# Optimization experiments

Hardware: AMD Instinct MI355X
Metric: run time of the kernel (lower is better)

The kernel has to match this reference:

```python
import jax, jax.numpy as jnp
import numpy as np

N, E, B = 524288, 4194304, 16384
F_IN, FP, TV, GOUT = 14, 1024, 256, 32
EPS = 1e-5
SLOPE = 0.2  # PyG GATConv default negative_slope


def setup_inputs() -> dict:
    key = jax.random.key(0)
    ks = iter(jax.random.split(key, 64))
    def nrm(shape, scale=1.0):
        return jax.random.normal(next(ks), shape, dtype=jnp.float32) * scale
    def uni(shape, lo, hi):
        return jax.random.uniform(next(ks), shape, dtype=jnp.float32, minval=lo, maxval=hi)
    def bn(d):  # [gamma, beta, running_mean, running_var]
        return jnp.stack([uni((d,), 0.5, 1.5), nrm((d,), 0.1), nrm((d,), 0.1), uni((d,), 0.5, 1.5)])
    return {
        'x': nrm((N, F_IN)),
        'edge_index': jax.random.randint(next(ks), (2, E), 0, N, dtype=jnp.int32),
        'batch': jnp.sort(jax.random.randint(next(ks), (N,), 0, B, dtype=jnp.int32)),
        'fingerprint': nrm((B, FP)),
        'transformer_features': nrm((B, TV)),
        'W1': nrm((F_IN, F_IN), 0.3), 'a_src1': nrm((F_IN,), 0.3), 'a_dst1': nrm((F_IN,), 0.3), 'b1': nrm((F_IN,), 0.1),
        'W2': nrm((F_IN, GOUT), 0.3), 'a_src2': nrm((GOUT,), 0.3), 'a_dst2': nrm((GOUT,), 0.3), 'b2': nrm((GOUT,), 0.1),
        'fc1_w': nrm((FP, 400), 0.04), 'fc1_b': nrm((400,), 0.1), 'bn1': bn(400),
        'fc2_w': nrm((400, 200), 0.07), 'fc2_b': nrm((200,), 0.1), 'bn2': bn(200),
        'fc3_w': nrm((TV, 400), 0.08), 'fc3_b': nrm((400,), 0.1), 'bn3': bn(400),
        'fc4_w': nrm((400, 200), 0.07), 'fc4_b': nrm((200,), 0.1), 'bn4': bn(200),
        'fcc1_w': nrm((GOUT + 400, 100), 0.07), 'fcc1_b': nrm((100,), 0.1), 'bnc': bn(100),
        'fcc2_w': nrm((100, 1), 0.1), 'fcc2_b': nrm((1,), 0.1),
    }


def _bn(h, p):  # eval-mode BatchNorm1d with packed params [4, d]
    return (h - p[2]) * jax.lax.rsqrt(p[3] + EPS) * p[0] + p[1]


def _gat(x, W, a_s, a_d, b, src, dst, n):
    # PyG GATConv, heads=1: messages flow src -> dst, softmax over incoming edges per dst
    h = x @ W                                   # [n, C]
    e = jax.nn.leaky_relu((h @ a_s)[src] + (h @ a_d)[dst], SLOPE)  # [E_tot]
    m = jax.lax.stop_gradient(jax.ops.segment_max(e, dst, num_segments=n))
    w = jnp.exp(e - m[dst])
    denom = jax.ops.segment_sum(w, dst, num_segments=n)
    alpha = w / denom[dst]
    out = jax.ops.segment_sum(alpha[:, None] * h[src], dst, num_segments=n)
    return out + b


def reference(x, edge_index, batch, fingerprint, transformer_features,
              W1, a_src1, a_dst1, b1, W2, a_src2, a_dst2, b2,
              fc1_w, fc1_b, bn1, fc2_w, fc2_b, bn2,
              fc3_w, fc3_b, bn3, fc4_w, fc4_b, bn4,
              fcc1_w, fcc1_b, bnc, fcc2_w, fcc2_b):
    n = x.shape[0]
    loop = jnp.arange(n, dtype=edge_index.dtype)  # add_self_loops
    src = jnp.concatenate([edge_index[0], loop])
    dst = jnp.concatenate([edge_index[1], loop])
    g = jax.nn.relu(_gat(x, W1, a_src1, a_dst1, b1, src, dst, n))
    g = jax.nn.relu(_gat(g, W2, a_src2, a_dst2, b2, src, dst, n))
    pool = jax.ops.segment_sum(g, batch, num_segments=B)  # global_add_pool -> [B, GOUT]
    fp = jax.nn.relu(_bn(fingerprint @ fc1_w + fc1_b, bn1))
    fp = jax.nn.relu(_bn(fp @ fc2_w + fc2_b, bn2))
    tv = jax.nn.relu(_bn(transformer_features @ fc3_w + fc3_b, bn3))
    tv = jax.nn.relu(_bn(tv @ fc4_w + fc4_b, bn4))
    comb = jnp.concatenate([pool, fp, tv], axis=1)  # [B, 32+200+200]
    comb = jax.nn.relu(_bn(comb @ fcc1_w + fcc1_b, bnc))
    return comb @ fcc2_w + fcc2_b  # [B, 1]
```

## Files before the change

### kernel.cpp

```cpp
#include <hip/hip_runtime.h>

typedef unsigned short u16;
typedef unsigned int u32;
typedef __attribute__((ext_vector_type(8))) short bf16x8;
typedef __attribute__((ext_vector_type(4))) float f32x4;

#define N_NODES 524288
#define N_EDGES 4194304
#define N_GRAPH 16384
#define P_BLOCKS 1024
#define BKTS 512
#define DPB 1024
#define CAP 8960
#define TTOT 2825

__device__ __forceinline__ float bf2f(u16 u){ u32 x=((u32)u)<<16; float f; __builtin_memcpy(&f,&x,4); return f; }
__device__ __forceinline__ float lo2f(u32 u){ u32 x=u<<16; float f; __builtin_memcpy(&f,&x,4); return f; }
__device__ __forceinline__ float hi2f(u32 u){ u32 x=u&0xffff0000u; float f; __builtin_memcpy(&f,&x,4); return f; }
__device__ __forceinline__ u16 f2bf(float f){ u32 x; __builtin_memcpy(&x,&f,4); return (u16)((x + 0x7fffu + ((x>>16)&1u))>>16); }
__device__ __forceinline__ float lrelu(float e){ return e>0.f? e : 0.2f*e; }
__device__ __forceinline__ float gload(const void* p, int i, int is32){
    return is32 ? ((const float*)p)[i] : bf2f(((const u16*)p)[i]);
}
__device__ __forceinline__ u32 fmax_key(float f){ u32 u; __builtin_memcpy(&u,&f,4); return (u>>31)? ~u : (u|0x80000000u); }
__device__ __forceinline__ float key_fmax(u32 k){ u32 u = (k>>31)? (k^0x80000000u) : ~k; float f; __builtin_memcpy(&f,&u,4); return f; }

__device__ __forceinline__ void edge_acc(uint4 q0, uint4 q1, float adv, float M,
        float* acc, float& den){
    float as_; __builtin_memcpy(&as_, &q1.w, 4);
    float w = __expf(lrelu(as_ + adv) - M); den += w;
    u32 u[7] = {q0.x,q0.y,q0.z,q0.w,q1.x,q1.y,q1.z};
    #pragma unroll
    for (int f=0;f<14;f++){ u32 uu=u[f>>1]; acc[f] += w*((f&1)? hi2f(uu):lo2f(uu)); }
}

__device__ __forceinline__ void walk8(const int* __restrict__ ssrc, const u16* __restrict__ hsrc,
        int beg, int end, float adv, float M, float* acc, float& den){
    for (int j = beg; j < end; j += 8){
        int s8[8];
        #pragma unroll
        for (int k=0;k<8;k++){
            int e = j + k;
            s8[k] = __builtin_nontemporal_load(ssrc + ((e < end) ? e : (end-1)));
        }
        uint4 r0[8], r1[8];
        #pragma unroll
        for (int k=0;k<8;k++){
            const uint4* hp = (const uint4*)(hsrc + (size_t)s8[k]*16);
            r0[k] = hp[0]; r1[k] = hp[1];
        }
        int m = end - j;
        #pragma unroll
        for (int k=0;k<8;k++) if (k < m) edge_acc(r0[k], r1[k], adv, M, acc, den);
    }
}

__device__ __forceinline__ void gemm_block(u16 (*As)[40], u16 (*Bs)[40],
        const void* __restrict__ A, const u16* __restrict__ Wt,
        const void* __restrict__ bias, const void* __restrict__ bnp, void* __restrict__ out,
        int K, int Kp, int Nc, int ostride, int ooff, int do_relu,
        int out32, int araw, int is32, int bm, int bn, int t){
    int af32 = araw && is32;
    int lane = t & 63, wave = t >> 6;
    int mt = (wave & 1) * 64, nt = (wave >> 1) * 64;
    int quad = lane >> 4, fr = lane & 15;

    f32x4 zero = {0.f, 0.f, 0.f, 0.f};
    f32x4 acc[4][4];
    #pragma unroll
    for (int i=0;i<4;i++)
        #pragma unroll
        for (int j=0;j<4;j++) acc[i][j] = zero;

    int srow0 = t >> 2;
    int scol = (t & 3) * 8;

    for (int k0 = 0; k0 < Kp; k0 += 32){
        #pragma unroll
        for (int h2_=0; h2_<2; h2_++){
            int row = srow0 + h2_*64;
            int gk = k0 + scol;
            uint4 av = make_uint4(0,0,0,0);
            if (gk + 8 <= K){
                if (af32){
                    const float* ap = (const float*)A + (size_t)(bm+row)*K + gk;
                    float4 a0 = *(const float4*)ap, a1 = *(const float4*)(ap+4);
                    av.x = (u32)f2bf(a0.x) | ((u32)f2bf(a0.y)<<16);
                    av.y = (u32)f2bf(a0.z) | ((u32)f2bf(a0.w)<<16);
                    av.z = (u32)f2bf(a1.x) | ((u32)f2bf(a1.y)<<16);
                    av.w = (u32)f2bf(a1.z) | ((u32)f2bf(a1.w)<<16);
                } else {
                    av = *(const uint4*)((const u16*)A + (size_t)(bm+row)*K + gk);
                }
            }
            *(uint4*)(&As[row][scol]) = av;
            uint4 bv = make_uint4(0,0,0,0);
            if (bn + row < Nc) bv = *(const uint4*)(Wt + (size_t)(bn+row)*Kp + gk);
            *(uint4*)(&Bs[row][scol]) = bv;
        }
        __syncthreads();
        bf16x8 af[4], bfr[4];
        #pragma unroll
        for (int i=0;i<4;i++) af[i] = *(const bf16x8*)(&As[mt + i*16 + fr][quad*8]);
        #pragma unroll
        for (int j=0;j<4;j++) bfr[j] = *(const bf16x8*)(&Bs[nt + j*16 + fr][quad*8]);
        #pragma unroll
        for (int i=0;i<4;i++)
            #pragma unroll
            for (int j=0;j<4;j++)
                acc[i][j] = __builtin_amdgcn_mfma_f32_16x16x32_bf16(af[i], bfr[j], acc[i][j], 0, 0, 0);
        __syncthreads();
    }

    #pragma unroll
    for (int j=0;j<4;j++){
        int gn = bn + nt + j*16 + fr;
        if (gn >= Nc) continue;
        float bb = gload(bias, gn, is32);
        float scale = 1.f, shift = bb;
        if (bnp){
            float gm_ = gload(bnp, gn, is32), bt = gload(bnp, Nc+gn, is32);
            float mn = gload(bnp, 2*Nc+gn, is32), vr = gload(bnp, 3*Nc+gn, is32);
            scale = gm_ * rsqrtf(vr + 1e-5f);
            shift = (bb - mn)*scale + bt;
        }
        #pragma unroll
        for (int i=0;i<4;i++){
            #pragma unroll
            for (int r=0;r<4;r++){
                int gm = bm + mt + i*16 + quad*4 + r;
                float v = acc[i][j][r]*scale + shift;
                if (do_relu) v = fmaxf(v, 0.f);
                size_t oidx = (size_t)gm*ostride + ooff + gn;
                if (out32) ((float*)out)[oidx] = v;
                else       ((u16*)out)[oidx] = f2bf(v);
            }
        }
    }
}

__global__ __launch_bounds__(256) void k_detect(const u32* __restrict__ x, int* __restrict__ flag,
        const void* __restrict__ W2, const void* __restrict__ asw, const void* __restrict__ adw,
        float* __restrict__ prep){
    __shared__ int cnt, s32;
    int t = threadIdx.x;
    if (t==0) cnt = 0;
    __syncthreads();
    int c = 0;
    for (int i = t; i < 1024; i += 256){
        u32 e = (x[i] >> 7) & 0xFF;
        if (e >= 110 && e <= 140) c++;
    }
    atomicAdd(&cnt, c);
    __syncthreads();
    if (t==0){ int f = (cnt < 512) ? 1 : 0; *flag = f; s32 = f; }
    __syncthreads();
    int is32 = s32;
    if (t < 28){
        int j = t % 14, which = t / 14;
        const void* av = which ? adw : asw;
        float s = 0.f;
        #pragma unroll
        for (int k=0;k<32;k++) s += gload(W2, j*32+k, is32) * gload(av, k, is32);
        prep[which*14 + j] = s;
    }
}

__global__ __launch_bounds__(256) void k_p1t(const int* __restrict__ dst, u32* __restrict__ tbl_bm,
        const void* __restrict__ Wa, const void* __restrict__ Wb, const void* __restrict__ Wc,
        const void* __restrict__ Wd, const void* __restrict__ We,
        u16* __restrict__ Ta, u16* __restrict__ Tb, u16* __restrict__ Tc,
        u16* __restrict__ Td, u16* __restrict__ Te, const int* __restrict__ flag){
    __shared__ u32 lh[BKTS];
    int bid = blockIdx.x, t = threadIdx.x;
    if (bid >= P_BLOCKS){
        int is32 = *flag;
        int loc = (bid - P_BLOCKS)*256 + t;
        const int n1=400*1024, n2=200*416, n3=400*256, n4=200*416, n5=100*448;
        const void* W; u16* T; int K, Kp, Nc;
        if (loc < n1){ W=Wa; T=Ta; K=1024; Kp=1024; Nc=400; }
        else if ((loc-=n1) < n2){ W=Wb; T=Tb; K=400; Kp=416; Nc=200; }
        else if ((loc-=n2) < n3){ W=Wc; T=Tc; K=256; Kp=256; Nc=400; }
        else if ((loc-=n3) < n4){ W=Wd; T=Td; K=400; Kp=416; Nc=200; }
        else if ((loc-=n4) < n5){ W=We; T=Te; K=432; Kp=448; Nc=100; }
        else return;
        int n = loc / Kp, k = loc - n*Kp;
        T[loc] = (k < K) ? f2bf(gload(W, k*Nc + n, is32)) : (u16)0;
        return;
    }
    int blk = bid;
    lh[t] = 0; lh[t+256] = 0;
    __syncthreads();
    int base = blk*4096;
    #pragma unroll
    for (int k=0;k<16;k++){
        int d = __builtin_nontemporal_load(dst + base + k*256 + t) & (N_NODES-1);
        atomicAdd(&lh[d>>10], 1);
    }
    __syncthreads();
    tbl_bm[blk*BKTS + t]       = lh[t];
    tbl_bm[blk*BKTS + t + 256] = lh[t+256];
}

__global__ __launch_bounds__(256) void k_ttbl(const u32* __restrict__ bm, u32* __restrict__ km){
    __shared__ u32 tile[32][33];
    int bx = blockIdx.x, by = blockIdx.y;
    int tx = threadIdx.x & 31, ty = threadIdx.x >> 5;
    #pragma unroll
    for (int r=0;r<32;r+=8)
        tile[ty+r][tx] = bm[(bx*32 + ty + r)*BKTS + by*32 + tx];
    __syncthreads();
    #pragma unroll
    for (int r=0;r<32;r+=8)
        km[(by*32 + ty + r)*P_BLOCKS + bx*32 + tx] = tile[tx][ty+r];
}

__global__ __launch_bounds__(256) void k_scan1(int* __restrict__ data, int* __restrict__ bsums){
    __shared__ int sh[256];
    int b = blockIdx.x, t = threadIdx.x;
    int base = b*1024 + t*4;
    int4 v = *(const int4*)(data + base);
    int s = v.x+v.y+v.z+v.w;
    sh[t] = s; __syncthreads();
    for (int off=1; off<256; off<<=1){
        int xv = (t>=off)? sh[t-off] : 0; __syncthreads();
        sh[t] += xv; __syncthreads();
    }
    int excl = sh[t] - s;
    if (t==255) bsums[b] = sh[255];
    int4 o; o.x = excl; o.y = excl+v.x; o.z = o.y+v.y; o.w = o.z+v.z;
    *(int4*)(data + base) = o;
}

__global__ __launch_bounds__(256) void k_scan2(int* __restrict__ bsums){
    __shared__ int sh[256];
    int t = threadIdx.x;
    int v0 = bsums[2*t], v1 = bsums[2*t+1];
    int s = v0+v1; sh[t] = s; __syncthreads();
    for (int off=1; off<256; off<<=1){
        int xv = (t>=off)? sh[t-off] : 0; __syncthreads();
        sh[t] += xv; __syncthreads();
    }
    int excl = sh[t] - s;
    bsums[2*t] = excl; bsums[2*t+1] = excl + v0;
}

__global__ __launch_bounds__(256) void k_scan3(int* __restrict__ scan, const int* __restrict__ bsums, int N_, int E_){
    int i = blockIdx.x*256 + threadIdx.x;
    if (i < N_) scan[i] += bsums[i>>10];
    if (i == 0) scan[N_] = E_;
}

__global__ __launch_bounds__(256) void k_p2(const int* __restrict__ src, const int* __restrict__ dst,
        const u32* __restrict__ km, u32* __restrict__ btab){
    __shared__ u32 lh[BKTS], lofs[BKTS], gofs[BKTS];
    __shared__ u32 stage[4096], tgt[4096];
    __shared__ u32 red[256];
    int t = threadIdx.x, blk = blockIdx.x;
    lh[t] = 0; lh[t+256] = 0;
    __syncthreads();
    u32 pr[16], rk[16]; u16 bk[16];
    int base = blk*4096;
    #pragma unroll
    for (int k=0;k<16;k++){
        int e = base + k*256 + t;
        int d = __builtin_nontemporal_load(dst+e) & (N_NODES-1);
        int s = __builtin_nontemporal_load(src+e) & (N_NODES-1);
        u32 b = (u32)d >> 10;
        bk[k] = (u16)b;
        pr[k] = (u32)(d & 1023) | ((u32)s << 10);
        rk[k] = atomicAdd(&lh[b], 1);
    }
    gofs[t]       = km[(size_t)t*P_BLOCKS + blk];
    gofs[t+256]   = km[(size_t)(t+256)*P_BLOCKS + blk];
    __syncthreads();
    u32 v0 = lh[2*t], v1 = lh[2*t+1];
    u32 s2 = v0+v1; red[t] = s2; __syncthreads();
    for (int off=1; off<256; off<<=1){
        u32 xv = (t>=off)? red[t-off] : 0; __syncthreads();
        red[t] += xv; __syncthreads();
    }
    u32 excl = red[t] - s2;
    lofs[2*t] = excl; lofs[2*t+1] = excl + v0;
    __syncthreads();
    #pragma unroll
    for (int k=0;k<16;k++){
        u32 p = lofs[bk[k]] + rk[k];
        stage[p] = pr[k];
        tgt[p]   = gofs[bk[k]] + rk[k];
    }
    __syncthreads();
    #pragma unroll
    for (int k=0;k<16;k++){
        int j = k*256 + t;
        btab[tgt[j]] = stage[j];
    }
}

__global__ __launch_bounds__(256) void k_p3(const u32* __restrict__ km, const u32* __restrict__ btab,
        int* __restrict__ rowptr, int* __restrict__ ssrc){
    __shared__ u32 fh[DPB], fo[DPB];
    __shared__ u32 red[256];
    __shared__ int sst[CAP];
    int t = threadIdx.x, b = blockIdx.x;
    u32 basep = km[(size_t)b*P_BLOCKS];
    u32 endp  = km[(size_t)(b+1)*P_BLOCKS];
    int cnt = (int)(endp - basep);
    #pragma unroll
    for (int i=t;i<DPB;i+=256) fh[i] = 0;
    __syncthreads();
    for (int j=t; j<cnt; j+=256){
        u32 p = btab[basep + j];
        atomicAdd(&fh[p & 1023], 1);
    }
    __syncthreads();
    u32 v0=fh[4*t], v1=fh[4*t+1], v2=fh[4*t+2], v3=fh[4*t+3];
    u32 s4 = v0+v1+v2+v3; red[t] = s4; __syncthreads();
    for (int off=1; off<256; off<<=1){
        u32 xv = (t>=off)? red[t-off] : 0; __syncthreads();
        red[t] += xv; __syncthreads();
    }
    u32 excl = red[t] - s4;
    fo[4*t]=excl; fo[4*t+1]=excl+v0; fo[4*t+2]=excl+v0+v1; fo[4*t+3]=excl+v0+v1+v2;
    __syncthreads();
    #pragma unroll
    for (int i=t;i<DPB;i+=256) rowptr[b*DPB + i] = (int)(basep + fo[i]);
    if (b == BKTS-1 && t == 0) rowptr[N_NODES] = (int)endp;
    __syncthreads();
    for (int j=t; j<cnt; j+=256){
        u32 p = btab[basep + j];
        u32 pos = atomicAdd(&fo[p & 1023], 1);
        if (pos < (u32)CAP) sst[pos] = (int)(p >> 10);
    }
    __syncthreads();
    for (int j=t; j<cnt; j+=256) ssrc[basep + j] = sst[j];
}

__global__ __launch_bounds__(256) void k_linear1(const void* __restrict__ x,
        const void* __restrict__ W1, const void* __restrict__ asw, const void* __restrict__ adw,
        u16* __restrict__ h1, float* __restrict__ ad1, u32* __restrict__ gkey,
        const int* __restrict__ flag){
    int is32 = *flag;
    __shared__ float Wf[196], av[14], dv[14];
    __shared__ float red[256];
    int t = threadIdx.x;
    if (t < 196) Wf[t] = gload(W1, t, is32);
    else if (t < 210) av[t-196] = gload(asw, t-196, is32);
    else if (t < 224) dv[t-210] = gload(adw, t-210, is32);
    __syncthreads();
    int i = blockIdx.x*256 + t;
    float xv[14];
    if (is32){
        const float* xr = (const float*)x + (size_t)i*14;
        #pragma unroll
        for (int k=0;k<14;k++) xv[k] = xr[k];
    } else {
        const u32* xr = (const u32*)((const u16*)x + (size_t)i*14);
        #pragma unroll
        for (int p=0;p<7;p++){ u32 u = xr[p]; xv[2*p]=lo2f(u); xv[2*p+1]=hi2f(u); }
    }
    float h[14];
    #pragma unroll
    for (int j=0;j<14;j++){ float s=0.f;
        #pragma unroll
        for (int k=0;k<14;k++) s += xv[k]*Wf[k*14+j];
        h[j]=s; }
    float a=0.f, d=0.f;
    #pragma unroll
    for (int j=0;j<14;j++){ a += h[j]*av[j]; d += h[j]*dv[j]; }
    ad1[i]=d;
    u32 ou[8];
    #pragma unroll
    for (int p=0;p<7;p++) ou[p] = (u32)f2bf(h[2*p]) | ((u32)f2bf(h[2*p+1])<<16);
    __builtin_memcpy(&ou[7], &a, 4);
    uint4* hp = (uint4*)(h1 + (size_t)i*16);
    hp[0] = make_uint4(ou[0],ou[1],ou[2],ou[3]);
    hp[1] = make_uint4(ou[4],ou[5],ou[6],ou[7]);
    red[t] = a; __syncthreads();
    for (int o=128;o;o>>=1){ if (t<o) red[t]=fmaxf(red[t],red[t+o]); __syncthreads(); }
    if (t==0) atomicMax(gkey, fmax_key(red[0]));
}

__global__ __launch_bounds__(256) void k_g1mlp(const int* __restrict__ rowptr, const int* __restrict__ ssrc,
        const u16* __restrict__ h1, const float* __restrict__ ad1, const u32* __restrict__ gkey1,
        const void* __restrict__ b1, const float* __restrict__ prep,
        u16* __restrict__ g1, float* __restrict__ ad2, u32* __restrict__ gkey2,
        const int* __restrict__ flag,
        const void* __restrict__ fing, const u16* __restrict__ Wt1,
        const void* __restrict__ fc1b, const void* __restrict__ bn1, u16* __restrict__ fp1,
        const void* __restrict__ tv, const u16* __restrict__ Wt3,
        const void* __restrict__ fc3b, const void* __restrict__ bn3, u16* __restrict__ tv1){
    __shared__ u16 As[128][40];
    __shared__ u16 Bs[128][40];
    __shared__ float b1s[14], vas[14], vds[14];
    __shared__ float red[256];
    int is32 = *flag;
    int bid = blockIdx.x, t = threadIdx.x;
    if (bid % 3 == 0){
        int g = bid / 3;
        int gg = (g < 512) ? g : g - 512;
        int r = gg & 7, q = gg >> 3;
        int bn = (q & 3) * 128;
        int bm = ((q >> 2) * 8 + r) * 128;
        if (g < 512)
            gemm_block(As, Bs, fing, Wt1, fc1b, bn1, fp1, 1024, 1024, 400, 400, 0, 1, 0,
                       1, is32, bm, bn, t);
        else
            gemm_block(As, Bs, tv, Wt3, fc3b, bn3, tv1, 256, 256, 400, 400, 0, 1, 0,
                       1, is32, bm, bn, t);
        return;
    }
    int gb = bid - bid/3 - 1;
    if (t < 14) b1s[t] = gload(b1, t, is32);
    else if (t < 28) vas[t-14] = prep[t-14];
    else if (t < 42) vds[t-28] = prep[t-28+14];
    __syncthreads();
    int i = gb*256 + t;
    float adv = ad1[i];
    float M = lrelu(key_fmax(*gkey1) + adv);
    int beg = rowptr[i], end = rowptr[i+1];
    float acc[14] = {0,0,0,0,0,0,0,0,0,0,0,0,0,0};
    float den = 0.f;
    {
        const uint4* hp = (const uint4*)(h1 + (size_t)i*16);
        edge_acc(hp[0], hp[1], adv, M, acc, den);
    }
    walk8(ssrc, h1, beg, end, adv, M, acc, den);
    float inv = 1.0f/den;
    float v[14];
    #pragma unroll
    for (int f=0;f<14;f++) v[f] = fmaxf(acc[f]*inv + b1s[f], 0.f);
    float a2=0.f, d2=0.f;
    #pragma unroll
    for (int f=0;f<14;f++){ a2 += v[f]*vas[f]; d2 += v[f]*vds[f]; }
    ad2[i] = d2;
    u32 ou[8];
    #pragma unroll
    for (int p=0;p<7;p++) ou[p] = (u32)f2bf(v[2*p]) | ((u32)f2bf(v[2*p+1])<<16);
    __builtin_memcpy(&ou[7], &a2, 4);
    uint4* gp = (uint4*)(g1 + (size_t)i*16);
    gp[0]=make_uint4(ou[0],ou[1],ou[2],ou[3]);
    gp[1]=make_uint4(ou[4],ou[5],ou[6],ou[7]);
    red[t] = a2; __syncthreads();
    for (int o=128;o;o>>=1){ if (t<o) red[t]=fmaxf(red[t],red[t+o]); __syncthreads(); }
    if (t==0) atomicMax(gkey2, fmax_key(red[0]));
}

__global__ __launch_bounds__(256) void k_g2mlp(const int* __restrict__ rowptr, const int* __restrict__ ssrc,
        const u16* __restrict__ g1, const float* __restrict__ ad2, const u32* __restrict__ gkey2,
        const void* __restrict__ W2, const void* __restrict__ b2, u16* __restrict__ g2,
        const int* __restrict__ flag,
        const u16* __restrict__ fp1, const u16* __restrict__ Wt2,
        const void* __restrict__ fc2b, const void* __restrict__ bn2,
        const u16* __restrict__ tv1, const u16* __restrict__ Wt4,
        const void* __restrict__ fc4b, const void* __restrict__ bn4,
        u16* __restrict__ comb){
    __shared__ u16 As[128][40];
    __shared__ u16 Bs[128][40];
    __shared__ float W2s[448], b2s[32];
    int is32 = *flag;
    int bid = blockIdx.x, t = threadIdx.x;
    if (bid % 5 == 0){
        int g = bid / 5;
        int gg = (g < 256) ? g : g - 256;
        int r = gg & 7, q = gg >> 3;
        int bn = (q & 1) * 128;
        int bm = ((q >> 1) * 8 + r) * 128;
        if (g < 256)
            gemm_block(As, Bs, fp1, Wt2, fc2b, bn2, comb, 400, 416, 200, 432, 32, 1, 0,
                       0, is32, bm, bn, t);
        else
            gemm_block(As, Bs, tv1, Wt4, fc4b, bn4, comb, 400, 416, 200, 432, 232, 1, 0,
                       0, is32, bm, bn, t);
        return;
    }
    int gb = bid - bid/5 - 1;
    for (int idx=t; idx<448; idx+=256) W2s[idx] = gload(W2, idx, is32);
    if (t < 32) b2s[t] = gload(b2, t, is32);
    __syncthreads();
    int i = gb*256 + t;
    float adv = ad2[i];
    float M = lrelu(key_fmax(*gkey2) + adv);
    int beg = rowptr[i], end = rowptr[i+1];
    float acc[14] = {0,0,0,0,0,0,0,0,0,0,0,0,0,0};
    float den = 0.f;
    {
        const uint4* hp = (const uint4*)(g1 + (size_t)i*16);
        edge_acc(hp[0], hp[1], adv, M, acc, den);
    }
    walk8(ssrc, g1, beg, end, adv, M, acc, den);
    float inv = 1.0f/den;
    float an[14];
    #pragma unroll
    for (int f=0;f<14;f++) an[f] = acc[f]*inv;
    uint4* orow = (uint4*)(g2 + (size_t)i*32);
    #pragma unroll
    for (int g=0; g<4; g++){
        u32 ou[4];
        #pragma unroll
        for (int p=0;p<4;p++){
            int j0 = g*8 + 2*p;
            float va_ = b2s[j0], vb_ = b2s[j0+1];
            #pragma unroll
            for (int k=0;k<14;k++){ va_ += an[k]*W2s[k*32+j0]; vb_ += an[k]*W2s[k*32+j0+1]; }
            va_ = fmaxf(va_, 0.f); vb_ = fmaxf(vb_, 0.f);
            ou[p] = (u32)f2bf(va_) | ((u32)f2bf(vb_)<<16);
        }
        orow[g] = make_uint4(ou[0],ou[1],ou[2],ou[3]);
    }
}

__device__ __forceinline__ int lbound(const int* __restrict__ a, int n, int v){
    int lo=0, hi=n;
    while (lo < hi){ int m = (lo+hi)>>1; if (a[m] < v) lo = m+1; else hi = m; }
    return lo;
}

__global__ __launch_bounds__(64) void k_pool(const u16* __restrict__ g2, const int* __restrict__ batch,
        u16* __restrict__ comb, int N_){
    int b = blockIdx.x;
    int t = threadIdx.x, f = t & 31, half = t >> 5;
    int lo = lbound(batch, N_, b);
    int hi = lbound(batch, N_, b+1);
    float acc = 0.f;
    for (int i = lo + half; i < hi; i += 2) acc += bf2f(g2[(size_t)i*32 + f]);
    acc += __shfl_xor(acc, 32);
    if (t < 32) comb[(size_t)b*432 + f] = f2bf(acc);
}

__global__ __launch_bounds__(256) void k_gemm(const void* __restrict__ A, const u16* __restrict__ Wt,
        const void* __restrict__ bias, const void* __restrict__ bnp, void* __restrict__ out,
        int K, int Kp, int Nc, int ostride, int ooff, int do_relu,
        int out32, int araw, const int* __restrict__ flag){
    __shared__ u16 As[128][40];
    __shared__ u16 Bs[128][40];
    int is32 = *flag;
    gemm_block(As, Bs, A, Wt, bias, bnp, out, K, Kp, Nc, ostride, ooff, do_relu, out32,
               araw, is32, blockIdx.x*128, blockIdx.y*128, threadIdx.x);
}

__global__ __launch_bounds__(256) void k_fcc2(const float* __restrict__ c1, const void* __restrict__ w,
        const void* __restrict__ b, float* __restrict__ outp, const int* __restrict__ flag){
    int is32 = *flag;
    __shared__ float wf[100];
    int t = threadIdx.x;
    if (t < 100) wf[t] = gload(w, t, is32);
    __syncthreads();
    int i = blockIdx.x*256 + t;
    const float* r = c1 + (size_t)i*100;
    float s = 0.f;
    #pragma unroll 4
    for (int k=0;k<100;k++) s += r[k]*wf[k];
    outp[i] = s + gload(b, 0, is32);
}

extern "C" void kernel_launch(void* const* d_in, const int* in_sizes, int n_in,
                              void* d_out, int out_size, void* d_ws, size_t ws_size,
                              hipStream_t stream){
    const int N = N_NODES, E = N_EDGES;
    const void* x    = d_in[0];
    const int* ei   = (const int*)d_in[1];
    const int* srcA = ei;
    const int* dstA = ei + E;
    const int* batch= (const int*)d_in[2];
    const void* fing = d_in[3];
    const void* tv   = d_in[4];
    const void* W1   = d_in[5];
    const void* as1w = d_in[6];
    const void* ad1w = d_in[7];
    const void* b1   = d_in[8];
    const void* W2   = d_in[9];
    const void* as2w = d_in[10];
    const void* ad2w = d_in[11];
    const void* b2   = d_in[12];
    const void* fc1w = d_in[13]; const void* fc1b = d_in[14]; const void* bn1 = d_in[15];
    const void* fc2w = d_in[16]; const void* fc2b = d_in[17]; const void* bn2 = d_in[18];
    const void* fc3w = d_in[19]; const void* fc3b = d_in[20]; const void* bn3 = d_in[21];
    const void* fc4w = d_in[22]; const void* fc4b = d_in[23]; const void* bn4 = d_in[24];
    const void* fccw = d_in[25]; const void* fccb = d_in[26]; const void* bnc = d_in[27];
    const void* fcc2w= d_in[28]; const void* fcc2b= d_in[29];

    char* ws = (char*)d_ws;
    size_t off = 0;
    auto alloc = [&](size_t bytes)->char*{ char* p = ws + off; off = (off + bytes + 255) & ~(size_t)255; return p; };
    int*  flagp  = (int*)alloc(256);
    u32*  gkey1  = (u32*)flagp + 1;
    u32*  gkey2  = (u32*)flagp + 2;
    float* prep  = (float*)((char*)flagp + 16);
    int*  rowptr = (int*)alloc((size_t)(N+1)*4);
    int*  bsums  = (int*)alloc(513*4);
    u32*  tbl_bm = (u32*)alloc((size_t)BKTS*P_BLOCKS*4);
    u32*  tbl_km = (u32*)alloc(((size_t)BKTS*P_BLOCKS+1)*4);
    int*  ssrc   = (int*)alloc((size_t)E*4);
    u16*  h1     = (u16*)alloc((size_t)N*16*2);
    u16*  g1     = (u16*)alloc((size_t)N*16*2);
    float* ad1_  = (float*)alloc((size_t)N*4);
    float* ad2_  = (float*)alloc((size_t)N*4);
    char* scr32  = alloc((size_t)N*32*2);
    float* c1    = (float*)alloc((size_t)N_GRAPH*100*4);
    u16*  Wt1    = (u16*)alloc((size_t)400*1024*2);
    u16*  Wt2    = (u16*)alloc((size_t)200*416*2);
    u16*  Wt3    = (u16*)alloc((size_t)400*256*2);
    u16*  Wt4    = (u16*)alloc((size_t)200*416*2);
    u16*  Wtc    = (u16*)alloc((size_t)100*448*2);
    u16*  fp1    = (u16*)alloc((size_t)N_GRAPH*400*2);
    u16*  tv1    = (u16*)alloc((size_t)N_GRAPH*400*2);
    u32*  btab   = (u32*)scr32;
    u16*  g2     = (u16*)scr32;
    u16*  comb   = (u16*)h1;

    (void)hipMemsetAsync(flagp, 0, 256, stream);

    k_detect <<<1, 256, 0, stream>>>((const u32*)x, flagp, W2, as2w, ad2w, prep);

    k_p1t  <<<P_BLOCKS + TTOT, 256, 0, stream>>>(dstA, tbl_bm,
                 fc1w, fc2w, fc3w, fc4w, fccw, Wt1, Wt2, Wt3, Wt4, Wtc, flagp);
    k_ttbl <<<dim3(32,16), 256, 0, stream>>>(tbl_bm, tbl_km);
    k_scan1<<<512,  256, 0, stream>>>((int*)tbl_km, bsums);
    k_scan2<<<1,    256, 0, stream>>>(bsums);
    k_scan3<<<(BKTS*P_BLOCKS)/256, 256, 0, stream>>>((int*)tbl_km, bsums, BKTS*P_BLOCKS, E);
    k_p2   <<<P_BLOCKS, 256, 0, stream>>>(srcA, dstA, tbl_km, btab);
    k_p3   <<<BKTS, 256, 0, stream>>>(tbl_km, btab, rowptr, ssrc);

    k_linear1<<<N/256, 256, 0, stream>>>(x, W1, as1w, ad1w, h1, ad1_, gkey1, flagp);
    k_g1mlp <<<3072, 256, 0, stream>>>(rowptr, ssrc, h1, ad1_, gkey1, b1, prep, g1, ad2_, gkey2, flagp,
                                       fing, Wt1, fc1b, bn1, fp1,
                                       tv,   Wt3, fc3b, bn3, tv1);
    k_g2mlp <<<2560, 256, 0, stream>>>(rowptr, ssrc, g1, ad2_, gkey2, W2, b2, g2, flagp,
                                       fp1, Wt2, fc2b, bn2,
                                       tv1, Wt4, fc4b, bn4, comb);
    k_pool   <<<N_GRAPH, 64, 0, stream>>>(g2, batch, comb, N);

    k_gemm<<<dim3(128,1), 256, 0, stream>>>(comb, Wtc, fccb, bnc, c1,  432, 448, 100, 100,   0, 1, 1, 0, flagp);

    k_fcc2<<<N_GRAPH/256, 256, 0, stream>>>(c1, fcc2w, fcc2b, (float*)d_out, flagp);
}
```

Before: 634.5 us.

## Fuse global add pool into GAT layer 2 and linear1 into partition kernel

Removes the separate k_pool kernel and the g2 buffer. Layer-2 GAT outputs are now summed directly into an fp32 comb buffer, using shared-memory atomics per block with a fallback to global atomics. The final fcc1 GEMM reads that buffer as raw fp32 through a new araw mode. The k_linear1 kernel is folded into the k_p1t launch as extra blocks, and a memset is added to zero comb32 first. This trades a kernel launch and a pass over the g2 buffer for float atomics, which make the summation order nondeterministic.

```diff
diff --git a/kernel.cpp b/kernel.cpp
--- a/kernel.cpp
+++ b/kernel.cpp
@@ -13,6 +13,7 @@
 #define DPB 1024
 #define CAP 8960
 #define TTOT 2825
+#define LBLK 2048
 
 __device__ __forceinline__ float bf2f(u16 u){ u32 x=((u32)u)<<16; float f; __builtin_memcpy(&f,&x,4); return f; }
 __device__ __forceinline__ float lo2f(u32 u){ u32 x=u<<16; float f; __builtin_memcpy(&f,&x,4); return f; }
@@ -60,7 +61,7 @@
         const void* __restrict__ bias, const void* __restrict__ bnp, void* __restrict__ out,
         int K, int Kp, int Nc, int ostride, int ooff, int do_relu,
         int out32, int araw, int is32, int bm, int bn, int t){
-    int af32 = araw && is32;
+    int af32 = (araw == 2) || (araw == 1 && is32);
     int lane = t & 63, wave = t >> 6;
     int mt = (wave & 1) * 64, nt = (wave >> 1) * 64;
     int quad = lane >> 4, fr = lane & 15;
@@ -170,9 +171,53 @@
         const void* __restrict__ Wa, const void* __restrict__ Wb, const void* __restrict__ Wc,
         const void* __restrict__ Wd, const void* __restrict__ We,
         u16* __restrict__ Ta, u16* __restrict__ Tb, u16* __restrict__ Tc,
-        u16* __restrict__ Td, u16* __restrict__ Te, const int* __restrict__ flag){
+        u16* __restrict__ Td, u16* __restrict__ Te, const int* __restrict__ flag,
+        const void* __restrict__ x, const void* __restrict__ W1,
+        const void* __restrict__ asw, const void* __restrict__ adw,
+        u16* __restrict__ h1, float* __restrict__ ad1, u32* __restrict__ gkey){
     __shared__ u32 lh[BKTS];
+    __shared__ float Wf[196], av14[14], dv14[14];
+    __shared__ float red[256];
     int bid = blockIdx.x, t = threadIdx.x;
+    if (bid >= P_BLOCKS + TTOT){
+        int is32 = *flag;
+        if (t < 196) Wf[t] = gload(W1, t, is32);
+        else if (t < 210) av14[t-196] = gload(asw, t-196, is32);
+        else if (t < 224) dv14[t-210] = gload(adw, t-210, is32);
+        __syncthreads();
+        int i = (bid - P_BLOCKS - TTOT)*256 + t;
+        float xv[14];
+        if (is32){
+            const float* xr = (const float*)x + (size_t)i*14;
+            #pragma unroll
+            for (int k=0;k<14;k++) xv[k] = xr[k];
+        } else {
+            const u32* xr = (const u32*)((const u16*)x + (size_t)i*14);
+            #pragma unroll
+            for (int p=0;p<7;p++){ u32 u = xr[p]; xv[2*p]=lo2f(u); xv[2*p+1]=hi2f(u); }
+        }
+        float h[14];
+        #pragma unroll
+        for (int j=0;j<14;j++){ float s=0.f;
+            #pragma unroll
+            for (int k=0;k<14;k++) s += xv[k]*Wf[k*14+j];
+            h[j]=s; }
+        float a=0.f, d=0.f;
+        #pragma unroll
+        for (int j=0;j<14;j++){ a += h[j]*av14[j]; d += h[j]*dv14[j]; }
+        ad1[i]=d;
+        u32 ou[8];
+        #pragma unroll
+        for (int p=0;p<7;p++) ou[p] = (u32)f2bf(h[2*p]) | ((u32)f2bf(h[2*p+1])<<16);
+        __builtin_memcpy(&ou[7], &a, 4);
+        uint4* hp = (uint4*)(h1 + (size_t)i*16);
+        hp[0] = make_uint4(ou[0],ou[1],ou[2],ou[3]);
+        hp[1] = make_uint4(ou[4],ou[5],ou[6],ou[7]);
+        red[t] = a; __syncthreads();
+        for (int o=128;o;o>>=1){ if (t<o) red[t]=fmaxf(red[t],red[t+o]); __syncthreads(); }
+        if (t==0) atomicMax(gkey, fmax_key(red[0]));
+        return;
+    }
     if (bid >= P_BLOCKS){
         int is32 = *flag;
         int loc = (bid - P_BLOCKS)*256 + t;
@@ -334,51 +379,6 @@
     }
     __syncthreads();
     for (int j=t; j<cnt; j+=256) ssrc[basep + j] = sst[j];
-}
-
-__global__ __launch_bounds__(256) void k_linear1(const void* __restrict__ x,
-        const void* __restrict__ W1, const void* __restrict__ asw, const void* __restrict__ adw,
-        u16* __restrict__ h1, float* __restrict__ ad1, u32* __restrict__ gkey,
-        const int* __restrict__ flag){
-    int is32 = *flag;
-    __shared__ float Wf[196], av[14], dv[14];
-    __shared__ float red[256];
-    int t = threadIdx.x;
-    if (t < 196) Wf[t] = gload(W1, t, is32);
-    else if (t < 210) av[t-196] = gload(asw, t-196, is32);
-    else if (t < 224) dv[t-210] = gload(adw, t-210, is32);
-    __syncthreads();
-    int i = blockIdx.x*256 + t;
-    float xv[14];
-    if (is32){
-        const float* xr = (const float*)x + (size_t)i*14;
-        #pragma unroll
-        for (int k=0;k<14;k++) xv[k] = xr[k];
-    } else {
-        const u32* xr = (const u32*)((const u16*)x + (size_t)i*14);
-        #pragma unroll
-        for (int p=0;p<7;p++){ u32 u = xr[p]; xv[2*p]=lo2f(u); xv[2*p+1]=hi2f(u); }
-    }
-    float h[14];
-    #pragma unroll
-    for (int j=0;j<14;j++){ float s=0.f;
-        #pragma unroll
-        for (int k=0;k<14;k++) s += xv[k]*Wf[k*14+j];
-        h[j]=s; }
-    float a=0.f, d=0.f;
-    #pragma unroll
-    for (int j=0;j<14;j++){ a += h[j]*av[j]; d += h[j]*dv[j]; }
-    ad1[i]=d;
-    u32 ou[8];
-    #pragma unroll
-    for (int p=0;p<7;p++) ou[p] = (u32)f2bf(h[2*p]) | ((u32)f2bf(h[2*p+1])<<16);
-    __builtin_memcpy(&ou[7], &a, 4);
-    uint4* hp = (uint4*)(h1 + (size_t)i*16);
-    hp[0] = make_uint4(ou[0],ou[1],ou[2],ou[3]);
-    hp[1] = make_uint4(ou[4],ou[5],ou[6],ou[7]);
-    red[t] = a; __syncthreads();
-    for (int o=128;o;o>>=1){ if (t<o) red[t]=fmaxf(red[t],red[t+o]); __syncthreads(); }
-    if (t==0) atomicMax(gkey, fmax_key(red[0]));
 }
 
 __global__ __launch_bounds__(256) void k_g1mlp(const int* __restrict__ rowptr, const int* __restrict__ ssrc,
@@ -448,16 +448,17 @@
 
 __global__ __launch_bounds__(256) void k_g2mlp(const int* __restrict__ rowptr, const int* __restrict__ ssrc,
         const u16* __restrict__ g1, const float* __restrict__ ad2, const u32* __restrict__ gkey2,
-        const void* __restrict__ W2, const void* __restrict__ b2, u16* __restrict__ g2,
-        const int* __restrict__ flag,
+        const void* __restrict__ W2, const void* __restrict__ b2,
+        const int* __restrict__ flag, const int* __restrict__ batch,
         const u16* __restrict__ fp1, const u16* __restrict__ Wt2,
         const void* __restrict__ fc2b, const void* __restrict__ bn2,
         const u16* __restrict__ tv1, const u16* __restrict__ Wt4,
         const void* __restrict__ fc4b, const void* __restrict__ bn4,
-        u16* __restrict__ comb){
+        float* __restrict__ comb32){
     __shared__ u16 As[128][40];
     __shared__ u16 Bs[128][40];
     __shared__ float W2s[448], b2s[32];
+    __shared__ float pools[32][32];
     int is32 = *flag;
     int bid = blockIdx.x, t = threadIdx.x;
     if (bid % 5 == 0){
@@ -467,16 +468,17 @@
         int bn = (q & 1) * 128;
         int bm = ((q >> 1) * 8 + r) * 128;
         if (g < 256)
-            gemm_block(As, Bs, fp1, Wt2, fc2b, bn2, comb, 400, 416, 200, 432, 32, 1, 0,
+            gemm_block(As, Bs, fp1, Wt2, fc2b, bn2, comb32, 400, 416, 200, 432, 32, 1, 1,
                        0, is32, bm, bn, t);
         else
-            gemm_block(As, Bs, tv1, Wt4, fc4b, bn4, comb, 400, 416, 200, 432, 232, 1, 0,
+            gemm_block(As, Bs, tv1, Wt4, fc4b, bn4, comb32, 400, 416, 200, 432, 232, 1, 1,
                        0, is32, bm, bn, t);
         return;
     }
     int gb = bid - bid/5 - 1;
     for (int idx=t; idx<448; idx+=256) W2s[idx] = gload(W2, idx, is32);
     if (t < 32) b2s[t] = gload(b2, t, is32);
+    for (int idx=t; idx<1024; idx+=256) ((float*)pools)[idx] = 0.f;
     __syncthreads();
     int i = gb*256 + t;
     float adv = ad2[i];
@@ -493,39 +495,26 @@
     float an[14];
     #pragma unroll
     for (int f=0;f<14;f++) an[f] = acc[f]*inv;
-    uint4* orow = (uint4*)(g2 + (size_t)i*32);
-    #pragma unroll
-    for (int g=0; g<4; g++){
-        u32 ou[4];
-        #pragma unroll
-        for (int p=0;p<4;p++){
-            int j0 = g*8 + 2*p;
-            float va_ = b2s[j0], vb_ = b2s[j0+1];
-            #pragma unroll
-            for (int k=0;k<14;k++){ va_ += an[k]*W2s[k*32+j0]; vb_ += an[k]*W2s[k*32+j0+1]; }
-            va_ = fmaxf(va_, 0.f); vb_ = fmaxf(vb_, 0.f);
-            ou[p] = (u32)f2bf(va_) | ((u32)f2bf(vb_)<<16);
-        }
-        orow[g] = make_uint4(ou[0],ou[1],ou[2],ou[3]);
-    }
-}
-
-__device__ __forceinline__ int lbound(const int* __restrict__ a, int n, int v){
-    int lo=0, hi=n;
-    while (lo < hi){ int m = (lo+hi)>>1; if (a[m] < v) lo = m+1; else hi = m; }
-    return lo;
-}
-
-__global__ __launch_bounds__(64) void k_pool(const u16* __restrict__ g2, const int* __restrict__ batch,
-        u16* __restrict__ comb, int N_){
-    int b = blockIdx.x;
-    int t = threadIdx.x, f = t & 31, half = t >> 5;
-    int lo = lbound(batch, N_, b);
-    int hi = lbound(batch, N_, b+1);
-    float acc = 0.f;
-    for (int i = lo + half; i < hi; i += 2) acc += bf2f(g2[(size_t)i*32 + f]);
-    acc += __shfl_xor(acc, 32);
-    if (t < 32) comb[(size_t)b*432 + f] = f2bf(acc);
+    int g0 = batch[gb*256];
+    int myb = batch[i];
+    int myg = myb - g0;
+    #pragma unroll
+    for (int f=0; f<32; f++){
+        float v_ = b2s[f];
+        #pragma unroll
+        for (int k=0;k<14;k++) v_ += an[k]*W2s[k*32+f];
+        v_ = fmaxf(v_, 0.f);
+        if (myg < 32) atomicAdd(&pools[myg][f], v_);
+        else          atomicAdd(&comb32[(size_t)myb*432 + f], v_);
+    }
+    __syncthreads();
+    int ng = batch[gb*256 + 255] - g0 + 1;
+    if (ng > 32) ng = 32;
+    for (int idx = t; idx < ng*32; idx += 256){
+        int g = idx >> 5, f = idx & 31;
+        float v_ = pools[g][f];
+        if (v_ != 0.f) atomicAdd(&comb32[(size_t)(g0+g)*432 + f], v_);
+    }
 }
 
 __global__ __launch_bounds__(256) void k_gemm(const void* __restrict__ A, const u16* __restrict__ Wt,
@@ -606,15 +595,15 @@
     u16*  fp1    = (u16*)alloc((size_t)N_GRAPH*400*2);
     u16*  tv1    = (u16*)alloc((size_t)N_GRAPH*400*2);
     u32*  btab   = (u32*)scr32;
-    u16*  g2     = (u16*)scr32;
-    u16*  comb   = (u16*)h1;
+    float* comb32= (float*)scr32;
 
     (void)hipMemsetAsync(flagp, 0, 256, stream);
 
     k_detect <<<1, 256, 0, stream>>>((const u32*)x, flagp, W2, as2w, ad2w, prep);
 
-    k_p1t  <<<P_BLOCKS + TTOT, 256, 0, stream>>>(dstA, tbl_bm,
-                 fc1w, fc2w, fc3w, fc4w, fccw, Wt1, Wt2, Wt3, Wt4, Wtc, flagp);
+    k_p1t  <<<P_BLOCKS + TTOT + LBLK, 256, 0, stream>>>(dstA, tbl_bm,
+                 fc1w, fc2w, fc3w, fc4w, fccw, Wt1, Wt2, Wt3, Wt4, Wtc, flagp,
+                 x, W1, as1w, ad1w, h1, ad1_, gkey1);
     k_ttbl <<<dim3(32,16), 256, 0, stream>>>(tbl_bm, tbl_km);
     k_scan1<<<512,  256, 0, stream>>>((int*)tbl_km, bsums);
     k_scan2<<<1,    256, 0, stream>>>(bsums);
@@ -622,16 +611,16 @@
     k_p2   <<<P_BLOCKS, 256, 0, stream>>>(srcA, dstA, tbl_km, btab);
     k_p3   <<<BKTS, 256, 0, stream>>>(tbl_km, btab, rowptr, ssrc);
 
-    k_linear1<<<N/256, 256, 0, stream>>>(x, W1, as1w, ad1w, h1, ad1_, gkey1, flagp);
+    (void)hipMemsetAsync(comb32, 0, (size_t)N_GRAPH*432*4, stream);
+
     k_g1mlp <<<3072, 256, 0, stream>>>(rowptr, ssrc, h1, ad1_, gkey1, b1, prep, g1, ad2_, gkey2, flagp,
                                        fing, Wt1, fc1b, bn1, fp1,
                                        tv,   Wt3, fc3b, bn3, tv1);
-    k_g2mlp <<<2560, 256, 0, stream>>>(rowptr, ssrc, g1, ad2_, gkey2, W2, b2, g2, flagp,
+    k_g2mlp <<<2560, 256, 0, stream>>>(rowptr, ssrc, g1, ad2_, gkey2, W2, b2, flagp, batch,
                                        fp1, Wt2, fc2b, bn2,
-                                       tv1, Wt4, fc4b, bn4, comb);
-    k_pool   <<<N_GRAPH, 64, 0, stream>>>(g2, batch, comb, N);
-
-    k_gemm<<<dim3(128,1), 256, 0, stream>>>(comb, Wtc, fccb, bnc, c1,  432, 448, 100, 100,   0, 1, 1, 0, flagp);
+                                       tv1, Wt4, fc4b, bn4, comb32);
+
+    k_gemm<<<dim3(128,1), 256, 0, stream>>>(comb32, Wtc, fccb, bnc, c1, 432, 448, 100, 100, 0, 1, 1, 2, flagp);
 
     k_fcc2<<<N_GRAPH/256, 256, 0, stream>>>(c1, fcc2w, fcc2b, (float*)d_out, flagp);
 }
```

Measured after the change: 708.5 us. +11.7%, slower.

## Replace two-level bucketed CSR build with global atomic counting sort

Applied to the files above, without the earlier changes.

Drops the per-block bucket histogram, transpose, bucket scatter and per-bucket local sort. CSR is now built from a direct global atomic histogram over destination nodes, a scan into rowptr and cursor, and an atomic-cursor placement of sources. The node linear layer is folded into the histogram launch. This cuts kernel launches and intermediate table traffic, but adds heavy global atomic contention and scattered writes, and edge order within each row becomes nondeterministic.

```diff
diff --git a/kernel.cpp b/kernel.cpp
--- a/kernel.cpp
+++ b/kernel.cpp
@@ -9,10 +9,8 @@
 #define N_EDGES 4194304
 #define N_GRAPH 16384
 #define P_BLOCKS 1024
-#define BKTS 512
-#define DPB 1024
-#define CAP 8960
 #define TTOT 2825
+#define LBLK 2048
 
 __device__ __forceinline__ float bf2f(u16 u){ u32 x=((u32)u)<<16; float f; __builtin_memcpy(&f,&x,4); return f; }
 __device__ __forceinline__ float lo2f(u32 u){ u32 x=u<<16; float f; __builtin_memcpy(&f,&x,4); return f; }
@@ -166,14 +164,27 @@
     }
 }
 
-__global__ __launch_bounds__(256) void k_p1t(const int* __restrict__ dst, u32* __restrict__ tbl_bm,
+__global__ __launch_bounds__(256) void k_histt(const int* __restrict__ dst, int* __restrict__ rowcnt,
         const void* __restrict__ Wa, const void* __restrict__ Wb, const void* __restrict__ Wc,
         const void* __restrict__ Wd, const void* __restrict__ We,
         u16* __restrict__ Ta, u16* __restrict__ Tb, u16* __restrict__ Tc,
-        u16* __restrict__ Td, u16* __restrict__ Te, const int* __restrict__ flag){
-    __shared__ u32 lh[BKTS];
+        u16* __restrict__ Td, u16* __restrict__ Te, const int* __restrict__ flag,
+        const void* __restrict__ x, const void* __restrict__ W1,
+        const void* __restrict__ asw, const void* __restrict__ adw,
+        u16* __restrict__ h1, float* __restrict__ ad1, u32* __restrict__ gkey){
+    __shared__ float Wf[196], av14[14], dv14[14];
+    __shared__ float red[256];
     int bid = blockIdx.x, t = threadIdx.x;
-    if (bid >= P_BLOCKS){
+    if (bid < P_BLOCKS){
+        int base = bid*4096;
+        #pragma unroll
+        for (int k=0;k<16;k++){
+            int d = __builtin_nontemporal_load(dst + base + k*256 + t) & (N_NODES-1);
+            atomicAdd(&rowcnt[d], 1);
+        }
+        return;
+    }
+    if (bid < P_BLOCKS + TTOT){
         int is32 = *flag;
         int loc = (bid - P_BLOCKS)*256 + t;
         const int n1=400*1024, n2=200*416, n3=400*256, n4=200*416, n5=100*448;
@@ -188,31 +199,42 @@
         T[loc] = (k < K) ? f2bf(gload(W, k*Nc + n, is32)) : (u16)0;
         return;
     }
-    int blk = bid;
-    lh[t] = 0; lh[t+256] = 0;
-    __syncthreads();
-    int base = blk*4096;
-    #pragma unroll
-    for (int k=0;k<16;k++){
-        int d = __builtin_nontemporal_load(dst + base + k*256 + t) & (N_NODES-1);
-        atomicAdd(&lh[d>>10], 1);
-    }
-    __syncthreads();
-    tbl_bm[blk*BKTS + t]       = lh[t];
-    tbl_bm[blk*BKTS + t + 256] = lh[t+256];
-}
-
-__global__ __launch_bounds__(256) void k_ttbl(const u32* __restrict__ bm, u32* __restrict__ km){
-    __shared__ u32 tile[32][33];
-    int bx = blockIdx.x, by = blockIdx.y;
-    int tx = threadIdx.x & 31, ty = threadIdx.x >> 5;
-    #pragma unroll
-    for (int r=0;r<32;r+=8)
-        tile[ty+r][tx] = bm[(bx*32 + ty + r)*BKTS + by*32 + tx];
-    __syncthreads();
-    #pragma unroll
-    for (int r=0;r<32;r+=8)
-        km[(by*32 + ty + r)*P_BLOCKS + bx*32 + tx] = tile[tx][ty+r];
+    int is32 = *flag;
+    if (t < 196) Wf[t] = gload(W1, t, is32);
+    else if (t < 210) av14[t-196] = gload(asw, t-196, is32);
+    else if (t < 224) dv14[t-210] = gload(adw, t-210, is32);
+    __syncthreads();
+    int i = (bid - P_BLOCKS - TTOT)*256 + t;
+    float xv[14];
+    if (is32){
+        const float* xr = (const float*)x + (size_t)i*14;
+        #pragma unroll
+        for (int k=0;k<14;k++) xv[k] = xr[k];
+    } else {
+        const u32* xr = (const u32*)((const u16*)x + (size_t)i*14);
+        #pragma unroll
+        for (int p=0;p<7;p++){ u32 u = xr[p]; xv[2*p]=lo2f(u); xv[2*p+1]=hi2f(u); }
+    }
+    float h[14];
+    #pragma unroll
+    for (int j=0;j<14;j++){ float s=0.f;
+        #pragma unroll
+        for (int k=0;k<14;k++) s += xv[k]*Wf[k*14+j];
+        h[j]=s; }
+    float a=0.f, d=0.f;
+    #pragma unroll
+    for (int j=0;j<14;j++){ a += h[j]*av14[j]; d += h[j]*dv14[j]; }
+    ad1[i]=d;
+    u32 ou[8];
+    #pragma unroll
+    for (int p=0;p<7;p++) ou[p] = (u32)f2bf(h[2*p]) | ((u32)f2bf(h[2*p+1])<<16);
+    __builtin_memcpy(&ou[7], &a, 4);
+    uint4* hp = (uint4*)(h1 + (size_t)i*16);
+    hp[0] = make_uint4(ou[0],ou[1],ou[2],ou[3]);
+    hp[1] = make_uint4(ou[4],ou[5],ou[6],ou[7]);
+    red[t] = a; __syncthreads();
+    for (int o=128;o;o>>=1){ if (t<o) red[t]=fmaxf(red[t],red[t+o]); __syncthreads(); }
+    if (t==0) atomicMax(gkey, fmax_key(red[0]));
 }
 
 __global__ __launch_bounds__(256) void k_scan1(int* __restrict__ data, int* __restrict__ bsums){
@@ -245,140 +267,29 @@
     bsums[2*t] = excl; bsums[2*t+1] = excl + v0;
 }
 
-__global__ __launch_bounds__(256) void k_scan3(int* __restrict__ scan, const int* __restrict__ bsums, int N_, int E_){
+__global__ __launch_bounds__(256) void k_scan3(int* __restrict__ scan, const int* __restrict__ bsums,
+        int* __restrict__ cursor, int N_, int E_){
     int i = blockIdx.x*256 + threadIdx.x;
-    if (i < N_) scan[i] += bsums[i>>10];
+    if (i < N_){
+        int v = scan[i] + bsums[i>>10];
+        scan[i] = v;
+        cursor[i] = v;
+    }
     if (i == 0) scan[N_] = E_;
 }
 
-__global__ __launch_bounds__(256) void k_p2(const int* __restrict__ src, const int* __restrict__ dst,
-        const u32* __restrict__ km, u32* __restrict__ btab){
-    __shared__ u32 lh[BKTS], lofs[BKTS], gofs[BKTS];
-    __shared__ u32 stage[4096], tgt[4096];
-    __shared__ u32 red[256];
+__global__ __launch_bounds__(256) void k_place(const int* __restrict__ src, const int* __restrict__ dst,
+        int* __restrict__ cursor, int* __restrict__ ssrc){
     int t = threadIdx.x, blk = blockIdx.x;
-    lh[t] = 0; lh[t+256] = 0;
-    __syncthreads();
-    u32 pr[16], rk[16]; u16 bk[16];
     int base = blk*4096;
     #pragma unroll
     for (int k=0;k<16;k++){
         int e = base + k*256 + t;
         int d = __builtin_nontemporal_load(dst+e) & (N_NODES-1);
         int s = __builtin_nontemporal_load(src+e) & (N_NODES-1);
-        u32 b = (u32)d >> 10;
-        bk[k] = (u16)b;
-        pr[k] = (u32)(d & 1023) | ((u32)s << 10);
-        rk[k] = atomicAdd(&lh[b], 1);
-    }
-    gofs[t]       = km[(size_t)t*P_BLOCKS + blk];
-    gofs[t+256]   = km[(size_t)(t+256)*P_BLOCKS + blk];
-    __syncthreads();
-    u32 v0 = lh[2*t], v1 = lh[2*t+1];
-    u32 s2 = v0+v1; red[t] = s2; __syncthreads();
-    for (int off=1; off<256; off<<=1){
-        u32 xv = (t>=off)? red[t-off] : 0; __syncthreads();
-        red[t] += xv; __syncthreads();
-    }
-    u32 excl = red[t] - s2;
-    lofs[2*t] = excl; lofs[2*t+1] = excl + v0;
-    __syncthreads();
-    #pragma unroll
-    for (int k=0;k<16;k++){
-        u32 p = lofs[bk[k]] + rk[k];
-        stage[p] = pr[k];
-        tgt[p]   = gofs[bk[k]] + rk[k];
-    }
-    __syncthreads();
-    #pragma unroll
-    for (int k=0;k<16;k++){
-        int j = k*256 + t;
-        btab[tgt[j]] = stage[j];
-    }
-}
-
-__global__ __launch_bounds__(256) void k_p3(const u32* __restrict__ km, const u32* __restrict__ btab,
-        int* __restrict__ rowptr, int* __restrict__ ssrc){
-    __shared__ u32 fh[DPB], fo[DPB];
-    __shared__ u32 red[256];
-    __shared__ int sst[CAP];
-    int t = threadIdx.x, b = blockIdx.x;
-    u32 basep = km[(size_t)b*P_BLOCKS];
-    u32 endp  = km[(size_t)(b+1)*P_BLOCKS];
-    int cnt = (int)(endp - basep);
-    #pragma unroll
-    for (int i=t;i<DPB;i+=256) fh[i] = 0;
-    __syncthreads();
-    for (int j=t; j<cnt; j+=256){
-        u32 p = btab[basep + j];
-        atomicAdd(&fh[p & 1023], 1);
-    }
-    __syncthreads();
-    u32 v0=fh[4*t], v1=fh[4*t+1], v2=fh[4*t+2], v3=fh[4*t+3];
-    u32 s4 = v0+v1+v2+v3; red[t] = s4; __syncthreads();
-    for (int off=1; off<256; off<<=1){
-        u32 xv = (t>=off)? red[t-off] : 0; __syncthreads();
-        red[t] += xv; __syncthreads();
-    }
-    u32 excl = red[t] - s4;
-    fo[4*t]=excl; fo[4*t+1]=excl+v0; fo[4*t+2]=excl+v0+v1; fo[4*t+3]=excl+v0+v1+v2;
-    __syncthreads();
-    #pragma unroll
-    for (int i=t;i<DPB;i+=256) rowptr[b*DPB + i] = (int)(basep + fo[i]);
-    if (b == BKTS-1 && t == 0) rowptr[N_NODES] = (int)endp;
-    __syncthreads();
-    for (int j=t; j<cnt; j+=256){
-        u32 p = btab[basep + j];
-        u32 pos = atomicAdd(&fo[p & 1023], 1);
-        if (pos < (u32)CAP) sst[pos] = (int)(p >> 10);
-    }
-    __syncthreads();
-    for (int j=t; j<cnt; j+=256) ssrc[basep + j] = sst[j];
-}
-
-__global__ __launch_bounds__(256) void k_linear1(const void* __restrict__ x,
-        const void* __restrict__ W1, const void* __restrict__ asw, const void* __restrict__ adw,
-        u16* __restrict__ h1, float* __restrict__ ad1, u32* __restrict__ gkey,
-        const int* __restrict__ flag){
-    int is32 = *flag;
-    __shared__ float Wf[196], av[14], dv[14];
-    __shared__ float red[256];
-    int t = threadIdx.x;
-    if (t < 196) Wf[t] = gload(W1, t, is32);
-    else if (t < 210) av[t-196] = gload(asw, t-196, is32);
-    else if (t < 224) dv[t-210] = gload(adw, t-210, is32);
-    __syncthreads();
-    int i = blockIdx.x*256 + t;
-    float xv[14];
-    if (is32){
-        const float* xr = (const float*)x + (size_t)i*14;
-        #pragma unroll
-        for (int k=0;k<14;k++) xv[k] = xr[k];
-    } else {
-        const u32* xr = (const u32*)((const u16*)x + (size_t)i*14);
-        #pragma unroll
-        for (int p=0;p<7;p++){ u32 u = xr[p]; xv[2*p]=lo2f(u); xv[2*p+1]=hi2f(u); }
-    }
-    float h[14];
-    #pragma unroll
-    for (int j=0;j<14;j++){ float s=0.f;
-        #pragma unroll
-        for (int k=0;k<14;k++) s += xv[k]*Wf[k*14+j];
-        h[j]=s; }
-    float a=0.f, d=0.f;
-    #pragma unroll
-    for (int j=0;j<14;j++){ a += h[j]*av[j]; d += h[j]*dv[j]; }
-    ad1[i]=d;
-    u32 ou[8];
-    #pragma unroll
-    for (int p=0;p<7;p++) ou[p] = (u32)f2bf(h[2*p]) | ((u32)f2bf(h[2*p+1])<<16);
-    __builtin_memcpy(&ou[7], &a, 4);
-    uint4* hp = (uint4*)(h1 + (size_t)i*16);
-    hp[0] = make_uint4(ou[0],ou[1],ou[2],ou[3]);
-    hp[1] = make_uint4(ou[4],ou[5],ou[6],ou[7]);
-    red[t] = a; __syncthreads();
-    for (int o=128;o;o>>=1){ if (t<o) red[t]=fmaxf(red[t],red[t+o]); __syncthreads(); }
-    if (t==0) atomicMax(gkey, fmax_key(red[0]));
+        int pos = atomicAdd(&cursor[d], 1);
+        ssrc[pos] = s;
+    }
 }
 
 __global__ __launch_bounds__(256) void k_g1mlp(const int* __restrict__ rowptr, const int* __restrict__ ssrc,
@@ -589,8 +500,7 @@
     float* prep  = (float*)((char*)flagp + 16);
     int*  rowptr = (int*)alloc((size_t)(N+1)*4);
     int*  bsums  = (int*)alloc(513*4);
-    u32*  tbl_bm = (u32*)alloc((size_t)BKTS*P_BLOCKS*4);
-    u32*  tbl_km = (u32*)alloc(((size_t)BKTS*P_BLOCKS+1)*4);
+    int*  cursor = (int*)alloc((size_t)N*4);
     int*  ssrc   = (int*)alloc((size_t)E*4);
     u16*  h1     = (u16*)alloc((size_t)N*16*2);
     u16*  g1     = (u16*)alloc((size_t)N*16*2);
@@ -605,24 +515,22 @@
     u16*  Wtc    = (u16*)alloc((size_t)100*448*2);
     u16*  fp1    = (u16*)alloc((size_t)N_GRAPH*400*2);
     u16*  tv1    = (u16*)alloc((size_t)N_GRAPH*400*2);
-    u32*  btab   = (u32*)scr32;
     u16*  g2     = (u16*)scr32;
     u16*  comb   = (u16*)h1;
 
     (void)hipMemsetAsync(flagp, 0, 256, stream);
+    (void)hipMemsetAsync(rowptr, 0, (size_t)(N+1)*4, stream);
 
     k_detect <<<1, 256, 0, stream>>>((const u32*)x, flagp, W2, as2w, ad2w, prep);
 
-    k_p1t  <<<P_BLOCKS + TTOT, 256, 0, stream>>>(dstA, tbl_bm,
-                 fc1w, fc2w, fc3w, fc4w, fccw, Wt1, Wt2, Wt3, Wt4, Wtc, flagp);
-    k_ttbl <<<dim3(32,16), 256, 0, stream>>>(tbl_bm, tbl_km);
-    k_scan1<<<512,  256, 0, stream>>>((int*)tbl_km, bsums);
+    k_histt <<<P_BLOCKS + TTOT + LBLK, 256, 0, stream>>>(dstA, rowptr,
+                 fc1w, fc2w, fc3w, fc4w, fccw, Wt1, Wt2, Wt3, Wt4, Wtc, flagp,
+                 x, W1, as1w, ad1w, h1, ad1_, gkey1);
+    k_scan1<<<512,  256, 0, stream>>>(rowptr, bsums);
     k_scan2<<<1,    256, 0, stream>>>(bsums);
-    k_scan3<<<(BKTS*P_BLOCKS)/256, 256, 0, stream>>>((int*)tbl_km, bsums, BKTS*P_BLOCKS, E);
-    k_p2   <<<P_BLOCKS, 256, 0, stream>>>(srcA, dstA, tbl_km, btab);
-    k_p3   <<<BKTS, 256, 0, stream>>>(tbl_km, btab, rowptr, ssrc);
-
-    k_linear1<<<N/256, 256, 0, stream>>>(x, W1, as1w, ad1w, h1, ad1_, gkey1, flagp);
+    k_scan3<<<N/256, 256, 0, stream>>>(rowptr, bsums, cursor, N, E);
+    k_place<<<P_BLOCKS, 256, 0, stream>>>(srcA, dstA, cursor, ssrc);
+
     k_g1mlp <<<3072, 256, 0, stream>>>(rowptr, ssrc, h1, ad1_, gkey1, b1, prep, g1, ad2_, gkey2, flagp,
                                        fing, Wt1, fc1b, bn1, fp1,
                                        tv,   Wt3, fc3b, bn3, tv1);
```

Result: slower. 1.034 ms (+62.9%).
